# Kernel optimization log

Hardware: AMD Instinct MI355X
Metric: run time of the kernel (lower is better)

## Reference

```python
import jax, jax.numpy as jnp
import numpy as np

VOCABSIZE = 100000
EMBEDSIZE = 128
BATCH = 262144


def setup_inputs() -> dict:
    key = jax.random.key(0)
    k1, k2, k3, k4, k5 = jax.random.split(key, 5)
    xs = jax.random.randint(k1, (BATCH,), 0, VOCABSIZE, dtype=jnp.int64 if jax.config.jax_enable_x64 else jnp.int32)
    ys = jax.random.randint(k2, (BATCH,), 0, VOCABSIZE, dtype=jnp.int64 if jax.config.jax_enable_x64 else jnp.int32)
    metric = jax.random.normal(k3, (EMBEDSIZE, EMBEDSIZE), dtype=jnp.float32)
    EMBEDM = jax.random.normal(k4, (VOCABSIZE, EMBEDSIZE), dtype=jnp.float32)
    # Original inits NEGEMBEDM to zeros; we use small random values so the
    # output / gradients are non-degenerate for kernel correctness testing.
    NEGEMBEDM = jax.random.normal(k5, (VOCABSIZE, EMBEDSIZE), dtype=jnp.float32) * 0.1
    return {"xs": xs, "ys": ys, "metric": metric, "EMBEDM": EMBEDM, "NEGEMBEDM": NEGEMBEDM}


def reference(xs, ys, metric, EMBEDM, NEGEMBEDM):
    # Faithful math: diag((E[xs] @ metric) @ N[ys].T) == sum((E[xs] @ metric) * N[ys], -1).
    # We compute the batched bilinear form directly, avoiding the O(B^2*D)
    # full matmul + diag extraction of the original.
    xsembeds = EMBEDM[xs]          # [B, D]
    ysembeds = NEGEMBEDM[ys]       # [B, D]
    d = jnp.einsum('bd,de,be->b', xsembeds, metric, ysembeds)  # [B]
    return jax.nn.sigmoid(2.0 * d - 1.0)
```

## Files before the change

### kernel.cpp

```cpp
#include <hip/hip_runtime.h>
#include <hip/hip_fp16.h>

#define D        128
#define NROWS    100000
#define NET      (NROWS / 16)
#define NNT      (NROWS / 4)
#define NUNITS   (NET + NNT)
#define GRID_P   1280
#define NWAVES   (GRID_P * 4)

typedef __attribute__((ext_vector_type(8))) _Float16 f16x8;
typedef __attribute__((ext_vector_type(4))) float    f32x4;

union F16x8U { _Float16 h[8]; f16x8 v; };
union F32x4U { float f[4]; f32x4 v; };

typedef __attribute__((address_space(1))) const void gvoid;
typedef __attribute__((address_space(3))) void       lvoid;

__global__ __launch_bounds__(256) void convert_M16(
    const float* __restrict__ M, _Float16* __restrict__ mh)
{
    const int q    = blockIdx.x * 256 + threadIdx.x;
    const int kk   = q >> 9;
    const int cf   = (q >> 6) & 7;
    const int lane = q & 63;
    const int col  = cf * 16 + (lane & 15);
    const int k0   = kk * 32 + (lane >> 4) * 8;

    F16x8U h;
    #pragma unroll
    for (int j = 0; j < 8; ++j) h.h[j] = (_Float16)M[(k0 + j) * D + col];
    *(f16x8*)(mh + q * 8) = h.v;
}

__global__ __launch_bounds__(256, 5) void prep_all(
    const float* __restrict__ E, const float* __restrict__ N,
    const _Float16* __restrict__ mh,
    _Float16* __restrict__ Ep, _Float16* __restrict__ Np)
{
    __shared__ _Float16 sm[2048 * 8];

    const int tid  = threadIdx.x;
    const int lane = tid & 63;
    const int w    = tid >> 6;
    const int lrow = lane & 15;
    const int lk   = lane >> 4;

    #pragma unroll
    for (int it = 0; it < 8; ++it) {
        const int slot = it * 256 + w * 64 + lane;
        __builtin_amdgcn_global_load_lds(
            (gvoid*)(mh + slot * 8), (lvoid*)(sm + (it * 256 + w * 64) * 8),
            16, 0, 0);
    }
    asm volatile("s_waitcnt vmcnt(0)" ::: "memory");
    __syncthreads();

    const f16x8* Bh = (const f16x8*)sm;

    const int gwave = (int)blockIdx.x * 4 + w;

    #pragma unroll 1
    for (int u = gwave; u < NUNITS; u += NWAVES) {
        if (u < NET) {
            const int row = u * 16 + lrow;

            f32x4 ax[4], ay[4];
            #pragma unroll
            for (int kk = 0; kk < 4; ++kk) {
                const float* p = E + (size_t)row * D + kk * 32 + lk * 8;
                ax[kk] = *(const f32x4*)p;
                ay[kk] = *(const f32x4*)(p + 4);
            }

            f32x4 acc[8];
            #pragma unroll
            for (int cf = 0; cf < 8; ++cf) acc[cf] = (f32x4){0.f, 0.f, 0.f, 0.f};

            #pragma unroll
            for (int kk = 0; kk < 4; ++kk) {
                F16x8U a16;
                F32x4U x, y; x.v = ax[kk]; y.v = ay[kk];
                #pragma unroll
                for (int j = 0; j < 4; ++j) {
                    a16.h[j]     = (_Float16)x.f[j];
                    a16.h[j + 4] = (_Float16)y.f[j];
                }
                #pragma unroll
                for (int cf = 0; cf < 8; ++cf)
                    acc[cf] = __builtin_amdgcn_mfma_f32_16x16x32_f16(
                        a16.v, Bh[(kk * 8 + cf) * 64 + lane], acc[cf], 0, 0, 0);
            }

            #pragma unroll
            for (int i = 0; i < 4; ++i) {
                const int ro = u * 16 + lk * 4 + i;
                F16x8U o;
                #pragma unroll
                for (int cf = 0; cf < 8; ++cf) o.h[cf] = (_Float16)acc[cf][i];
                *(f16x8*)(Ep + (size_t)ro * D + lrow * 8) = o.v;
            }
        } else {
            const int row = (u - NET) * 4 + lk;
            const float* src = N + (size_t)row * D + lrow;
            F16x8U o;
            #pragma unroll
            for (int k = 0; k < 8; ++k) o.h[k] = (_Float16)src[16 * k];
            *(f16x8*)(Np + (size_t)row * D + lrow * 8) = o.v;
        }
    }
}

__global__ __launch_bounds__(256) void gather_dot16(
    const int* __restrict__ xs, const int* __restrict__ ys,
    const _Float16* __restrict__ Ep, const _Float16* __restrict__ Np,
    float* __restrict__ out)
{
    const int tid = threadIdx.x;
    const int o0  = blockIdx.x * 32 + (tid >> 4) * 2;
    const int l   = tid & 15;

    const int x0 = xs[o0], x1 = xs[o0 + 1];
    const int y0 = ys[o0], y1 = ys[o0 + 1];

    const f16x8 a0 = *(const f16x8*)(Ep + (size_t)x0 * D + l * 8);
    const f16x8 b0 = *(const f16x8*)(Np + (size_t)y0 * D + l * 8);
    const f16x8 a1 = *(const f16x8*)(Ep + (size_t)x1 * D + l * 8);
    const f16x8 b1 = *(const f16x8*)(Np + (size_t)y1 * D + l * 8);

    float r0 = 0.f, r1 = 0.f;
    #pragma unroll
    for (int j = 0; j < 8; ++j) {
        r0 += (float)a0[j] * (float)b0[j];
        r1 += (float)a1[j] * (float)b1[j];
    }

    r0 += __shfl_xor(r0, 1); r1 += __shfl_xor(r1, 1);
    r0 += __shfl_xor(r0, 2); r1 += __shfl_xor(r1, 2);
    r0 += __shfl_xor(r0, 4); r1 += __shfl_xor(r1, 4);
    r0 += __shfl_xor(r0, 8); r1 += __shfl_xor(r1, 8);

    if (l == 0) {
        float2 v;
        v.x = 1.0f / (1.0f + __expf(1.0f - 2.0f * r0));
        v.y = 1.0f / (1.0f + __expf(1.0f - 2.0f * r1));
        *(float2*)(out + o0) = v;
    }
}

extern "C" void kernel_launch(void* const* d_in, const int* in_sizes, int n_in,
                              void* d_out, int out_size, void* d_ws, size_t ws_size,
                              hipStream_t stream) {
    const int*   xs     = (const int*)d_in[0];
    const int*   ys     = (const int*)d_in[1];
    const float* metric = (const float*)d_in[2];
    const float* EMBEDM = (const float*)d_in[3];
    const float* NEGEM  = (const float*)d_in[4];
    float*       out    = (float*)d_out;

    const int B = in_sizes[0];

    char* ws = (char*)d_ws;
    _Float16* Np = (_Float16*)ws;
    _Float16* Ep = (_Float16*)(ws + (32u << 20));
    _Float16* mh = (_Float16*)(ws + (64u << 20));

    convert_M16<<<8, 256, 0, stream>>>(metric, mh);

    prep_all<<<GRID_P, 256, 0, stream>>>(EMBEDM, NEGEM, mh, Ep, Np);

    gather_dot16<<<B / 32, 256, 0, stream>>>(xs, ys, Ep, Np, out);
}
```

Baseline: 53.07 us.

## Stage E and N row tiles through per-wave LDS with coalesced loads

The prep kernel now loads E and N rows with fully coalesced float4 reads into a per-wave LDS scratch buffer. E tiles are stored XOR-swizzled for MFMA operand reads, and N tiles are permuted in LDS before coalesced 16-byte stores. Work units are rebalanced so E and N tiles interleave, and the grid and occupancy hint are reduced to fit the extra LDS. This targets the strided global reads of the old N permutation and the scattered E operand loads, at the cost of LDS traffic, scalar 2-byte LDS stores that may bank-conflict, and lower occupancy.

```diff
diff --git a/kernel.cpp b/kernel.cpp
--- a/kernel.cpp
+++ b/kernel.cpp
@@ -4,15 +4,16 @@
 #define D        128
 #define NROWS    100000
 #define NET      (NROWS / 16)
-#define NNT      (NROWS / 4)
-#define NUNITS   (NET + NNT)
-#define GRID_P   1280
+#define NUNITS   (2 * NET)
+#define GRID_P   768
 #define NWAVES   (GRID_P * 4)
 
 typedef __attribute__((ext_vector_type(8))) _Float16 f16x8;
+typedef __attribute__((ext_vector_type(4))) _Float16 f16x4;
 typedef __attribute__((ext_vector_type(4))) float    f32x4;
 
 union F16x8U { _Float16 h[8]; f16x8 v; };
+union F16x4U { _Float16 h[4]; f16x4 v; };
 union F32x4U { float f[4]; f32x4 v; };
 
 typedef __attribute__((address_space(1))) const void gvoid;
@@ -34,12 +35,13 @@
     *(f16x8*)(mh + q * 8) = h.v;
 }
 
-__global__ __launch_bounds__(256, 5) void prep_all(
+__global__ __launch_bounds__(256, 3) void prep_all2(
     const float* __restrict__ E, const float* __restrict__ N,
     const _Float16* __restrict__ mh,
     _Float16* __restrict__ Ep, _Float16* __restrict__ Np)
 {
-    __shared__ _Float16 sm[2048 * 8];
+    __shared__ _Float16 smM[2048 * 8];
+    __shared__ _Float16 scr[4][2048];
 
     const int tid  = threadIdx.x;
     const int lane = tid & 63;
@@ -51,28 +53,36 @@
     for (int it = 0; it < 8; ++it) {
         const int slot = it * 256 + w * 64 + lane;
         __builtin_amdgcn_global_load_lds(
-            (gvoid*)(mh + slot * 8), (lvoid*)(sm + (it * 256 + w * 64) * 8),
+            (gvoid*)(mh + slot * 8), (lvoid*)(smM + (it * 256 + w * 64) * 8),
             16, 0, 0);
     }
     asm volatile("s_waitcnt vmcnt(0)" ::: "memory");
     __syncthreads();
 
-    const f16x8* Bh = (const f16x8*)sm;
+    const f16x8* Bh = (const f16x8*)smM;
+    _Float16*    S  = scr[w];
 
-    const int gwave = (int)blockIdx.x * 4 + w;
+    const int gw = (int)blockIdx.x * 4 + w;
 
     #pragma unroll 1
-    for (int u = gwave; u < NUNITS; u += NWAVES) {
-        if (u < NET) {
-            const int row = u * 16 + lrow;
+    for (int u = gw; u < NUNITS; u += NWAVES) {
+        const int t16 = u >> 1;
 
-            f32x4 ax[4], ay[4];
+        if ((u & 1) == 0) {
             #pragma unroll
-            for (int kk = 0; kk < 4; ++kk) {
-                const float* p = E + (size_t)row * D + kk * 32 + lk * 8;
-                ax[kk] = *(const f32x4*)p;
-                ay[kk] = *(const f32x4*)(p + 4);
+            for (int i = 0; i < 8; ++i) {
+                const int f   = i * 256 + lane * 4;
+                const int row = f >> 7;
+                const int col = f & 127;
+                F32x4U v; v.v = *(const f32x4*)(E + (size_t)t16 * 2048 + f);
+                F16x4U h4;
+                h4.h[0] = (_Float16)v.f[0]; h4.h[1] = (_Float16)v.f[1];
+                h4.h[2] = (_Float16)v.f[2]; h4.h[3] = (_Float16)v.f[3];
+                const int tsl = (col >> 3) ^ row;
+                *(f16x4*)(S + row * 128 + tsl * 8 + (col & 7)) = h4.v;
             }
+            asm volatile("s_waitcnt lgkmcnt(0)" ::: "memory");
+            __builtin_amdgcn_sched_barrier(0);
 
             f32x4 acc[8];
             #pragma unroll
@@ -80,35 +90,47 @@
 
             #pragma unroll
             for (int kk = 0; kk < 4; ++kk) {
-                F16x8U a16;
-                F32x4U x, y; x.v = ax[kk]; y.v = ay[kk];
-                #pragma unroll
-                for (int j = 0; j < 4; ++j) {
-                    a16.h[j]     = (_Float16)x.f[j];
-                    a16.h[j + 4] = (_Float16)y.f[j];
-                }
+                const f16x8 a16 =
+                    *(const f16x8*)(S + lrow * 128 + ((kk * 4 + lk) ^ lrow) * 8);
                 #pragma unroll
                 for (int cf = 0; cf < 8; ++cf)
                     acc[cf] = __builtin_amdgcn_mfma_f32_16x16x32_f16(
-                        a16.v, Bh[(kk * 8 + cf) * 64 + lane], acc[cf], 0, 0, 0);
+                        a16, Bh[(kk * 8 + cf) * 64 + lane], acc[cf], 0, 0, 0);
             }
 
             #pragma unroll
             for (int i = 0; i < 4; ++i) {
-                const int ro = u * 16 + lk * 4 + i;
+                const int ro = t16 * 16 + lk * 4 + i;
                 F16x8U o;
                 #pragma unroll
                 for (int cf = 0; cf < 8; ++cf) o.h[cf] = (_Float16)acc[cf][i];
                 *(f16x8*)(Ep + (size_t)ro * D + lrow * 8) = o.v;
             }
         } else {
-            const int row = (u - NET) * 4 + lk;
-            const float* src = N + (size_t)row * D + lrow;
-            F16x8U o;
             #pragma unroll
-            for (int k = 0; k < 8; ++k) o.h[k] = (_Float16)src[16 * k];
-            *(f16x8*)(Np + (size_t)row * D + lrow * 8) = o.v;
+            for (int i = 0; i < 8; ++i) {
+                const int f   = i * 256 + lane * 4;
+                const int row = f >> 7;
+                const int col = f & 127;
+                F32x4U v; v.v = *(const f32x4*)(N + (size_t)t16 * 2048 + f);
+                const int lo = col & 15;
+                const int hi = col >> 4;
+                _Float16* base = S + row * 128 + hi;
+                base[(lo    ) * 8] = (_Float16)v.f[0];
+                base[(lo + 1) * 8] = (_Float16)v.f[1];
+                base[(lo + 2) * 8] = (_Float16)v.f[2];
+                base[(lo + 3) * 8] = (_Float16)v.f[3];
+            }
+            asm volatile("s_waitcnt lgkmcnt(0)" ::: "memory");
+            __builtin_amdgcn_sched_barrier(0);
+
+            #pragma unroll
+            for (int i = 0; i < 4; ++i) {
+                const f16x8 t = *(const f16x8*)(S + i * 512 + lane * 8);
+                *(f16x8*)(Np + (size_t)t16 * 2048 + i * 512 + lane * 8) = t;
+            }
         }
+
     }
 }
 
@@ -168,7 +190,7 @@
 
     convert_M16<<<8, 256, 0, stream>>>(metric, mh);
 
-    prep_all<<<GRID_P, 256, 0, stream>>>(EMBEDM, NEGEM, mh, Ep, Np);
+    prep_all2<<<GRID_P, 256, 0, stream>>>(EMBEDM, NEGEM, mh, Ep, Np);
 
     gather_dot16<<<B / 32, 256, 0, stream>>>(xs, ys, Ep, Np, out);
 }
```

New measurement: 52.09 us. No clear change (-1.9%).
